# Kernel tuning notes

Hardware: AMD Instinct MI355X
Metric: run time of the kernel (lower is better)

Reference implementation:

```python
import jax, jax.numpy as jnp
import numpy as np
from jax import lax

HEADS = 8
EPS = 1e-5
B, HP, N = 16, 16, 256  # batch, patches per side, tokens


def _ln(x, w, b):
    m = x.mean(-1, keepdims=True)
    v = ((x - m) ** 2).mean(-1, keepdims=True)
    return (x - m) / jnp.sqrt(v + EPS) * w + b


def _mlp_block(x, n2w, n2b, f1w, f1b, f2w, f2b):
    h = _ln(x, n2w, n2b)
    h = jax.nn.gelu(h @ f1w.T + f1b, approximate=False)  # torch nn.GELU = exact erf
    return x + (h @ f2w.T + f2b)


def _stem_stage(x, params):
    def step(c, p):
        return _mlp_block(c, *p), None
    x, _ = lax.scan(step, x, params)
    return x


def _patch_merge(x, nw, nb, rw):
    # x: [B, N, s, s, C] -> [B, N, s/2, s/2, 2C]
    x = jnp.concatenate([x[..., 0::2, 0::2, :], x[..., 1::2, 0::2, :],
                         x[..., 0::2, 1::2, :], x[..., 1::2, 1::2, :]], axis=-1)
    return _ln(x, nw, nb) @ rw.T


def _main_block(x, p, rpe_index):
    n1w, n1b, qkvw, qkvb, rpb, pw, pb, n2w, n2b, f1w, f1b, f2w, f2b = p
    Bc, Nc, C = x.shape
    Dh = C // HEADS
    h = _ln(x, n1w, n1b)
    qkv = (h @ qkvw.T + qkvb).reshape(Bc, Nc, 3, HEADS, Dh)
    q, k, v = jnp.moveaxis(qkv, 2, 0)
    attn = jnp.einsum('bnhd,bmhd->bhnm', q * (Dh ** -0.5), k)
    # learned relative position bias gathered per (query, key) pair
    bias = rpb[rpe_index].reshape(Nc, Nc, HEADS).transpose(2, 0, 1)  # [H,N,N]
    attn = jax.nn.softmax((attn + bias[None]).astype(jnp.float32), axis=-1).astype(x.dtype)
    o = jnp.einsum('bhnm,bmhd->bnhd', attn, v).reshape(Bc, Nc, C)
    x = x + (o @ pw.T + pb)
    return _mlp_block(x, n2w, n2b, f1w, f1b, f2w, f2b)


def _forward(x, patch_w, patch_b, pnorm_w, pnorm_b,
             s0_n2w, s0_n2b, s0_fc1w, s0_fc1b, s0_fc2w, s0_fc2b,
             m0_nw, m0_nb, m0_rw,
             s1_n2w, s1_n2b, s1_fc1w, s1_fc1b, s1_fc2w, s1_fc2b,
             m1_nw, m1_nb, m1_rw, pos_embed,
             mb_n1w, mb_n1b, mb_qkvw, mb_qkvb, mb_rpb, mb_projw, mb_projb,
             mb_n2w, mb_n2b, mb_fc1w, mb_fc1b, mb_fc2w, mb_fc2b,
             fnorm_w, fnorm_b, rpe_index):
    Bc = x.shape[0]
    # PatchEmbed: 4x4/stride4 conv, regroup into [B, 256 patches, 4, 4, 128]
    h = lax.conv_general_dilated(x, patch_w, (4, 4), 'VALID',
                                 dimension_numbers=('NCHW', 'OIHW', 'NCHW'))
    h = h + patch_b[None, :, None, None]  # [B,128,64,64]
    h = h.reshape(Bc, 128, HP, 4, HP, 4).transpose(0, 2, 4, 3, 5, 1).reshape(Bc, N, 4, 4, 128)
    h = _ln(h, pnorm_w, pnorm_b)
    # stem stage 0 (8 MLP-only blocks, dim 128) + merge -> dim 256
    h = _stem_stage(h, (s0_n2w, s0_n2b, s0_fc1w, s0_fc1b, s0_fc2w, s0_fc2b))
    h = _patch_merge(h, m0_nw, m0_nb, m0_rw)  # [B,256,2,2,256]
    # stem stage 1 (8 MLP-only blocks, dim 256) + merge -> dim 512
    h = _stem_stage(h, (s1_n2w, s1_n2b, s1_fc1w, s1_fc1b, s1_fc2w, s1_fc2b))
    h = _patch_merge(h, m1_nw, m1_nb, m1_rw)  # [B,256,1,1,512]
    h = h[..., 0, 0, :] + pos_embed  # [B,256,512]
    # 20 main attention blocks with RPE
    def step(c, p):
        return _main_block(c, p, rpe_index), None
    h, _ = lax.scan(step, h, (mb_n1w, mb_n1b, mb_qkvw, mb_qkvb, mb_rpb,
                              mb_projw, mb_projb, mb_n2w, mb_n2b,
                              mb_fc1w, mb_fc1b, mb_fc2w, mb_fc2b))
    return _ln(h, fnorm_w, fnorm_b)


def _rpe_index():
    coords = np.stack(np.meshgrid(np.arange(HP), np.arange(HP), indexing='ij')).reshape(2, -1)
    rel = (coords[:, :, None] - coords[:, None, :]).transpose(1, 2, 0) + (HP - 1)
    return jnp.asarray((rel[..., 0] * (2 * HP - 1) + rel[..., 1]).reshape(-1), jnp.int32)


def setup_inputs() -> dict:
    key = jax.random.key(0)
    ks = iter(jax.random.split(key, 64))
    w = lambda shape: jax.random.normal(next(ks), shape, jnp.float32) * 0.02
    return {
        'x': jax.random.normal(next(ks), (B, 3, 256, 256), jnp.float32),
        'patch_w': w((128, 3, 4, 4)), 'patch_b': jnp.zeros(128),
        'pnorm_w': jnp.ones(128), 'pnorm_b': jnp.zeros(128),
        's0_n2w': jnp.ones((8, 128)), 's0_n2b': jnp.zeros((8, 128)),
        's0_fc1w': w((8, 384, 128)), 's0_fc1b': jnp.zeros((8, 384)),
        's0_fc2w': w((8, 128, 384)), 's0_fc2b': jnp.zeros((8, 128)),
        'm0_nw': jnp.ones(512), 'm0_nb': jnp.zeros(512), 'm0_rw': w((256, 512)),
        's1_n2w': jnp.ones((8, 256)), 's1_n2b': jnp.zeros((8, 256)),
        's1_fc1w': w((8, 768, 256)), 's1_fc1b': jnp.zeros((8, 768)),
        's1_fc2w': w((8, 256, 768)), 's1_fc2b': jnp.zeros((8, 256)),
        'm1_nw': jnp.ones(1024), 'm1_nb': jnp.zeros(1024), 'm1_rw': w((512, 1024)),
        'pos_embed': w((1, N, 512)),
        'mb_n1w': jnp.ones((20, 512)), 'mb_n1b': jnp.zeros((20, 512)),
        'mb_qkvw': w((20, 1536, 512)), 'mb_qkvb': jnp.zeros((20, 1536)),
        'mb_rpb': w((20, 961, 8)),
        'mb_projw': w((20, 512, 512)), 'mb_projb': jnp.zeros((20, 512)),
        'mb_n2w': jnp.ones((20, 512)), 'mb_n2b': jnp.zeros((20, 512)),
        'mb_fc1w': w((20, 2048, 512)), 'mb_fc1b': jnp.zeros((20, 2048)),
        'mb_fc2w': w((20, 512, 2048)), 'mb_fc2b': jnp.zeros((20, 512)),
        'fnorm_w': jnp.ones(512), 'fnorm_b': jnp.zeros(512),
        'rpe_index': _rpe_index(),
    }


def reference(x, patch_w, patch_b, pnorm_w, pnorm_b,
              s0_n2w, s0_n2b, s0_fc1w, s0_fc1b, s0_fc2w, s0_fc2b,
              m0_nw, m0_nb, m0_rw,
              s1_n2w, s1_n2b, s1_fc1w, s1_fc1b, s1_fc2w, s1_fc2b,
              m1_nw, m1_nb, m1_rw, pos_embed,
              mb_n1w, mb_n1b, mb_qkvw, mb_qkvb, mb_rpb, mb_projw, mb_projb,
              mb_n2w, mb_n2b, mb_fc1w, mb_fc1b, mb_fc2w, mb_fc2b,
              fnorm_w, fnorm_b, rpe_index):
    return _forward(x, patch_w, patch_b, pnorm_w, pnorm_b,
                    s0_n2w, s0_n2b, s0_fc1w, s0_fc1b, s0_fc2w, s0_fc2b,
                    m0_nw, m0_nb, m0_rw,
                    s1_n2w, s1_n2b, s1_fc1w, s1_fc1b, s1_fc2w, s1_fc2b,
                    m1_nw, m1_nb, m1_rw, pos_embed,
                    mb_n1w, mb_n1b, mb_qkvw, mb_qkvb, mb_rpb, mb_projw, mb_projb,
                    mb_n2w, mb_n2b, mb_fc1w, mb_fc1b, mb_fc2w, mb_fc2b,
                    fnorm_w, fnorm_b, rpe_index)
```

## Files before the change

### kernel.cpp

```cpp
#include <hip/hip_runtime.h>
#include <math.h>

#define EPSV 1e-5f

typedef __attribute__((ext_vector_type(8))) short bf16x8;
typedef __attribute__((ext_vector_type(4))) float f32x4;
typedef unsigned short ushort;

__device__ inline ushort f2bf(float x) {
  unsigned u = __builtin_bit_cast(unsigned, x);
  u += 0x7FFFu + ((u >> 16) & 1u);
  return (ushort)(u >> 16);
}

#define GLOAD16(lptr, gptr)                                              \
  __builtin_amdgcn_global_load_lds(                                      \
      (const __attribute__((address_space(1))) unsigned int*)(gptr),     \
      (__attribute__((address_space(3))) unsigned int*)(lptr), 16, 0, 0)

__global__ __launch_bounds__(256) void convh_kernel(
    const float* __restrict__ in, ushort* __restrict__ hi, int n4) {
  int i = blockIdx.x * 256 + threadIdx.x;
  if (i >= n4) return;
  float4 v = ((const float4*)in)[i];
  float vv[4] = {v.x, v.y, v.z, v.w};
  unsigned hw[4];
#pragma unroll
  for (int e = 0; e < 4; ++e) hw[e] = f2bf(vv[e]);
  ((uint2*)hi)[i] = make_uint2(hw[0] | (hw[1] << 16), hw[2] | (hw[3] << 16));
}

__global__ __launch_bounds__(256) void convmain_kernel(
    const float* __restrict__ src, ushort* __restrict__ dst, int perLayer4,
    int dstOff4, int n4) {
  int i = blockIdx.x * 256 + threadIdx.x;
  if (i >= n4) return;
  int l = i / perLayer4;
  int r = i - l * perLayer4;
  float4 v = ((const float4*)src)[i];
  float vv[4] = {v.x, v.y, v.z, v.w};
  unsigned hw[4];
#pragma unroll
  for (int e = 0; e < 4; ++e) hw[e] = f2bf(vv[e]);
  ((uint2*)dst)[(size_t)l * 786432 + dstOff4 + r] =
      make_uint2(hw[0] | (hw[1] << 16), hw[2] | (hw[3] << 16));
}

__global__ __launch_bounds__(256) void patch_ln2_kernel(
    const float* __restrict__ x, const float* __restrict__ pw,
    const float* __restrict__ pbias, const float* __restrict__ nw,
    const float* __restrict__ nb, float* __restrict__ out) {
  int bid = blockIdx.x;
  int b = bid >> 8, n = bid & 255;
  int py = (n >> 4) * 16, px0 = (n & 15) * 16;
  __shared__ float xin[3][16][16];
  __shared__ float wls[128][52];
  __shared__ float pbs[128];
  int tid = threadIdx.x;
  if (tid < 192) {
    int ci = tid / 64, rr = (tid % 64) >> 2, c4 = tid & 3;
    const float* src =
        x + ((size_t)(b * 3 + ci) * 256 + (py + rr)) * 256 + px0 + c4 * 4;
    *(float4*)&xin[ci][rr][c4 * 4] = *(const float4*)src;
  }
  for (int idx = tid; idx < 6144; idx += 256) {
    int c = idx / 48, q = idx % 48;
    wls[c][q] = pw[c * 48 + q];
  }
  if (tid < 128) pbs[tid] = pbias[tid];
  __syncthreads();

  int tt = tid >> 4, cg = tid & 15;
  int ii = tt >> 2, jj = tt & 3;
  float xv[48];
#pragma unroll
  for (int ci = 0; ci < 3; ++ci)
#pragma unroll
    for (int dy = 0; dy < 4; ++dy)
#pragma unroll
      for (int dx = 0; dx < 4; ++dx)
        xv[ci * 16 + dy * 4 + dx] = xin[ci][ii * 4 + dy][jj * 4 + dx];

  float o[8];
#pragma unroll
  for (int e = 0; e < 8; ++e) {
    int c = cg + e * 16;
    float a = pbs[c];
#pragma unroll
    for (int q4 = 0; q4 < 12; ++q4) {
      float4 w4 = *(const float4*)&wls[c][q4 * 4];
      a += w4.x * xv[q4 * 4] + w4.y * xv[q4 * 4 + 1] + w4.z * xv[q4 * 4 + 2] +
           w4.w * xv[q4 * 4 + 3];
    }
    o[e] = a;
  }
  float s = 0.f;
#pragma unroll
  for (int e = 0; e < 8; ++e) s += o[e];
#pragma unroll
  for (int off = 8; off > 0; off >>= 1) s += __shfl_xor(s, off, 16);
  float mean = s * (1.0f / 128.0f);
  float sq = 0.f;
#pragma unroll
  for (int e = 0; e < 8; ++e) {
    float d = o[e] - mean;
    sq += d * d;
  }
#pragma unroll
  for (int off = 8; off > 0; off >>= 1) sq += __shfl_xor(sq, off, 16);
  float rstd = rsqrtf(sq * (1.0f / 128.0f) + EPSV);
  size_t base = ((size_t)bid * 16 + tt) * 128;
#pragma unroll
  for (int e = 0; e < 8; ++e) {
    int c = cg + e * 16;
    out[base + c] = (o[e] - mean) * rstd * nw[c] + nb[c];
  }
}

template <int C>
__global__ __launch_bounds__(256) void lnC_kernel(
    const float* __restrict__ X, const float* __restrict__ w,
    const float* __restrict__ bb, ushort* __restrict__ outH) {
  constexpr int NV = C / 64;
  int wave = threadIdx.x >> 6, lane = threadIdx.x & 63;
  int row = blockIdx.x * 4 + wave;
  const float* xr = X + (size_t)row * C + lane * NV;
  float v[NV];
  if (NV == 2) {
    float2 t2 = *(const float2*)xr;
    v[0] = t2.x; v[1] = t2.y;
  } else {
#pragma unroll
    for (int q = 0; q < NV; q += 4) {
      float4 t4 = *(const float4*)(xr + q);
      v[q] = t4.x; v[q + 1] = t4.y; v[q + 2] = t4.z; v[q + 3] = t4.w;
    }
  }
  float s = 0.f;
#pragma unroll
  for (int q = 0; q < NV; ++q) s += v[q];
#pragma unroll
  for (int o = 32; o > 0; o >>= 1) s += __shfl_xor(s, o, 64);
  float mean = s * (1.0f / C);
  float sq = 0.f;
#pragma unroll
  for (int q = 0; q < NV; ++q) {
    float d = v[q] - mean;
    sq += d * d;
  }
#pragma unroll
  for (int o = 32; o > 0; o >>= 1) sq += __shfl_xor(sq, o, 64);
  float rstd = rsqrtf(sq * (1.0f / C) + EPSV);
#pragma unroll
  for (int q = 0; q < NV; ++q) {
    int c = lane * NV + q;
    outH[(size_t)row * C + c] = f2bf((v[q] - mean) * rstd * w[c] + bb[c]);
  }
}

template <int MODE>
__global__ __launch_bounds__(256) void merge_ln_kernel(
    const float* __restrict__ Xin, const float* __restrict__ nw,
    const float* __restrict__ nb, ushort* __restrict__ outH) {
  constexpr int CM = MODE ? 1024 : 512;
  constexpr int NE = CM / 256;
  int ot = blockIdx.x;
  int tid = threadIdx.x;
  __shared__ float redA[4];
  __shared__ float redB[4];

  float v[NE];
#pragma unroll
  for (int e = 0; e < NE; ++e) {
    int cp = tid + e * 256;
    if (MODE == 0) {
      int b = ot >> 10, r = ot & 1023;
      int n = r >> 2, di = (r >> 1) & 1, dj = r & 1;
      int q = cp >> 7, c = cp & 127;
      int i = 2 * di + (q & 1), j = 2 * dj + (q >> 1);
      v[e] = Xin[((b * 256 + n) * 16 + i * 4 + j) * 128 + c];
    } else {
      int b = ot >> 8, n = ot & 255;
      int q = cp >> 8, c = cp & 255;
      int di = q & 1, dj = q >> 1;
      v[e] = Xin[((b * 256 + n) * 4 + di * 2 + dj) * 256 + c];
    }
  }
  float s = 0.f;
#pragma unroll
  for (int e = 0; e < NE; ++e) s += v[e];
#pragma unroll
  for (int o = 32; o > 0; o >>= 1) s += __shfl_xor(s, o, 64);
  if ((tid & 63) == 0) redA[tid >> 6] = s;
  __syncthreads();
  float mean = (redA[0] + redA[1] + redA[2] + redA[3]) * (1.0f / CM);
  float sq = 0.f;
#pragma unroll
  for (int e = 0; e < NE; ++e) {
    float d = v[e] - mean;
    sq += d * d;
  }
#pragma unroll
  for (int o = 32; o > 0; o >>= 1) sq += __shfl_xor(sq, o, 64);
  if ((tid & 63) == 0) redB[tid >> 6] = sq;
  __syncthreads();
  float var = (redB[0] + redB[1] + redB[2] + redB[3]) * (1.0f / CM);
  float rstd = rsqrtf(var + EPSV);
#pragma unroll
  for (int e = 0; e < NE; ++e) {
    int cp = tid + e * 256;
    outH[(size_t)ot * CM + cp] = f2bf((v[e] - mean) * rstd * nw[cp] + nb[cp]);
  }
}

template <int EP, int BM>
__global__ __launch_bounds__(256) void mgemm4_kernel(
    const ushort* __restrict__ Ah, const ushort* __restrict__ Wh,
    const float* __restrict__ bias, const float* __restrict__ extra,
    float* __restrict__ outF, ushort* __restrict__ outH, int M, int N, int K) {
  constexpr int NI = BM / 32;
  constexpr int ASH = BM * 64;
  constexpr int LSZ = (ASH + 8192 > BM * 136) ? (ASH + 8192) : (BM * 136);
  __shared__ __align__(16) ushort Lds[LSZ];
  int nb = N >> 7;
  int bx = blockIdx.x % nb, by = blockIdx.x / nb;
  int tid = threadIdx.x;
  int wv = tid >> 6, lane = tid & 63;
  int srow = tid >> 3;
  int scol = ((tid & 7) ^ (srow & 7)) << 3;
  const ushort* aS = Ah + (size_t)(by * BM + srow) * K + scol;
  const ushort* wS = Wh + (size_t)(bx * 128 + srow) * K + scol;
  ushort* dA = Lds + wv * 512;
  ushort* dW = Lds + ASH + wv * 512;

  int wm = (wv >> 1) * (BM / 2), wn = (wv & 1) * 64;
  int fr = lane & 15, fq = lane >> 4;
  int rsw = fr & 7;

  f32x4 acc[NI][4];
#pragma unroll
  for (int i = 0; i < NI; ++i)
#pragma unroll
    for (int j = 0; j < 4; ++j) acc[i][j] = {0.f, 0.f, 0.f, 0.f};

  for (int k0 = 0; k0 < K; k0 += 64) {
#pragma unroll
    for (int q = 0; q < BM / 32; ++q)
      GLOAD16(dA + q * 2048, aS + (size_t)q * 32 * K + k0);
#pragma unroll
    for (int q = 0; q < 4; ++q)
      GLOAD16(dW + q * 2048, wS + (size_t)q * 32 * K + k0);
    __syncthreads();

#pragma unroll
    for (int kh = 0; kh < 2; ++kh) {
      bf16x8 fa[NI], fb[4];
#pragma unroll
      for (int i = 0; i < NI; ++i) {
        int row = wm + i * 16 + fr;
        fa[i] = *(const bf16x8*)(Lds + row * 64 + ((((kh << 2) + fq) ^ rsw) << 3));
      }
#pragma unroll
      for (int j = 0; j < 4; ++j) {
        int row = wn + j * 16 + fr;
        fb[j] = *(const bf16x8*)(Lds + ASH + row * 64 +
                                 ((((kh << 2) + fq) ^ rsw) << 3));
      }
#pragma unroll
      for (int i = 0; i < NI; ++i)
#pragma unroll
        for (int j = 0; j < 4; ++j)
          acc[i][j] = __builtin_amdgcn_mfma_f32_16x16x32_bf16(fa[i], fb[j],
                                                              acc[i][j], 0, 0,
                                                              0);
    }
    __syncthreads();
  }

  int row0 = by * BM;
  int col0 = bx * 128;
  if (EP == 3 || EP == 4) {
    ushort* LdsO = Lds;
#pragma unroll
    for (int j = 0; j < 4; ++j) {
      int col = wn + j * 16 + fr;
      float bvv = bias ? bias[col0 + col] : 0.f;
      bool sc = (EP == 4) && (col0 + col < 512);
#pragma unroll
      for (int i = 0; i < NI; ++i) {
#pragma unroll
        for (int e = 0; e < 4; ++e) {
          int rl = wm + i * 16 + fq * 4 + e;
          float o = acc[i][j][e] + bvv;
          if (EP == 3)
            o = 0.5f * o * (1.0f + erff(o * 0.70710678118654752f));
          else if (sc)
            o *= 0.125f;
          LdsO[rl * 136 + col] = f2bf(o);
        }
      }
    }
    __syncthreads();
#pragma unroll
    for (int p = 0; p < BM / 16; ++p) {
      int ch = p * 256 + tid;
      int r = ch >> 4, cc = (ch & 15) * 8;
      *(uint4*)&outH[(size_t)(row0 + r) * N + col0 + cc] =
          *(const uint4*)&LdsO[r * 136 + cc];
    }
  } else {
    float* LdsF = (float*)Lds;
    int strip = wv >> 1;
#pragma unroll
    for (int i = 0; i < NI; ++i) {
#pragma unroll
      for (int j = 0; j < 4; ++j) {
        int col = wn + j * 16 + fr;
        float bvv = bias ? bias[col0 + col] : 0.f;
#pragma unroll
        for (int e = 0; e < 4; ++e)
          LdsF[(strip * 16 + fq * 4 + e) * 136 + col] = acc[i][j][e] + bvv;
      }
      __syncthreads();
#pragma unroll
      for (int p = 0; p < 4; ++p) {
        int c = p * 256 + tid;
        int st = c >> 9;
        int rem = c & 511;
        int r = rem >> 5, cc = (rem & 31) * 4;
        int grow = row0 + st * (BM / 2) + i * 16 + r;
        float4 v = *(const float4*)&LdsF[(st * 16 + r) * 136 + cc];
        if (EP == 1) {
          float4 e4 =
              *(const float4*)&extra[(size_t)(grow & 255) * N + col0 + cc];
          v.x += e4.x; v.y += e4.y; v.z += e4.z; v.w += e4.w;
        } else if (EP == 2) {
          float4 e4 = *(const float4*)&extra[(size_t)grow * N + col0 + cc];
          v.x += e4.x; v.y += e4.y; v.z += e4.z; v.w += e4.w;
        }
        *(float4*)&outF[(size_t)grow * N + col0 + cc] = v;
      }
      __syncthreads();
    }
  }
}

__global__ __launch_bounds__(256) void attn_score_kernel(
    const ushort* __restrict__ qkvh, const float* __restrict__ rpb,
    const int* __restrict__ rpe, ushort* __restrict__ P) {
  int bid = blockIdx.x;
  int qc = bid & 3, bh = bid >> 2;
  int b = bh >> 3, h = bh & 7;
  int n0 = qc * 64;
  int tid = threadIdx.x;
  int wv = tid >> 6, lane = tid & 63;
  int fr = lane & 15, fq = lane >> 4;
  __shared__ __align__(16) ushort Qs[64 * 64];
  __shared__ __align__(16) ushort Ks[256 * 64];
  __shared__ float rpbh[961];
  __shared__ float red[64][4];

  int srow = tid >> 3;
  int sc = ((tid & 7) ^ (srow & 7)) << 3;
  const ushort* Qg = qkvh + (size_t)(b * 256 + n0 + srow) * 1536 + h * 64 + sc;
  GLOAD16(Qs + wv * 512, Qg);
  GLOAD16(Qs + 2048 + wv * 512, Qg + (size_t)32 * 1536);
  const ushort* Kg = qkvh + (size_t)(b * 256 + srow) * 1536 + 512 + h * 64 + sc;
#pragma unroll
  for (int q = 0; q < 8; ++q)
    GLOAD16(Ks + q * 2048 + wv * 512, Kg + (size_t)q * 32 * 1536);
  for (int i = tid; i < 961; i += 256) rpbh[i] = rpb[i * 8 + h];
  __syncthreads();

  f32x4 acc[4][4];
#pragma unroll
  for (int i = 0; i < 4; ++i)
#pragma unroll
    for (int j = 0; j < 4; ++j) acc[i][j] = {0.f, 0.f, 0.f, 0.f};
#pragma unroll
  for (int kh = 0; kh < 2; ++kh) {
    bf16x8 fa[4], fb[4];
#pragma unroll
    for (int i = 0; i < 4; ++i) {
      int row = i * 16 + fr;
      fa[i] = *(const bf16x8*)(Qs + row * 64 +
                               ((((kh << 2) + fq) ^ (row & 7)) << 3));
    }
#pragma unroll
    for (int j = 0; j < 4; ++j) {
      int row = wv * 64 + j * 16 + fr;
      fb[j] = *(const bf16x8*)(Ks + row * 64 +
                               ((((kh << 2) + fq) ^ (row & 7)) << 3));
    }
#pragma unroll
    for (int i = 0; i < 4; ++i)
#pragma unroll
      for (int j = 0; j < 4; ++j)
        acc[i][j] = __builtin_amdgcn_mfma_f32_16x16x32_bf16(fa[i], fb[j],
                                                            acc[i][j], 0, 0, 0);
  }

  float sreg[4][4][4];
#pragma unroll
  for (int i = 0; i < 4; ++i)
#pragma unroll
    for (int e = 0; e < 4; ++e) {
      int n = n0 + i * 16 + fq * 4 + e;
#pragma unroll
      for (int j = 0; j < 4; ++j) {
        int m = wv * 64 + j * 16 + fr;
        sreg[i][j][e] = acc[i][j][e] + rpbh[rpe[n * 256 + m]];
      }
    }

  float rmax[4][4];
#pragma unroll
  for (int i = 0; i < 4; ++i)
#pragma unroll
    for (int e = 0; e < 4; ++e) {
      float mx = fmaxf(fmaxf(sreg[i][0][e], sreg[i][1][e]),
                       fmaxf(sreg[i][2][e], sreg[i][3][e]));
#pragma unroll
      for (int o = 8; o > 0; o >>= 1) mx = fmaxf(mx, __shfl_xor(mx, o, 16));
      if (fr == 0) red[i * 16 + fq * 4 + e][wv] = mx;
    }
  __syncthreads();
#pragma unroll
  for (int i = 0; i < 4; ++i)
#pragma unroll
    for (int e = 0; e < 4; ++e) {
      int row = i * 16 + fq * 4 + e;
      rmax[i][e] = fmaxf(fmaxf(red[row][0], red[row][1]),
                         fmaxf(red[row][2], red[row][3]));
    }
  __syncthreads();
  float rinv[4][4];
#pragma unroll
  for (int i = 0; i < 4; ++i)
#pragma unroll
    for (int e = 0; e < 4; ++e) {
      float sm = 0.f;
#pragma unroll
      for (int j = 0; j < 4; ++j) {
        sreg[i][j][e] = expf(sreg[i][j][e] - rmax[i][e]);
        sm += sreg[i][j][e];
      }
#pragma unroll
      for (int o = 8; o > 0; o >>= 1) sm += __shfl_xor(sm, o, 16);
      if (fr == 0) red[i * 16 + fq * 4 + e][wv] = sm;
    }
  __syncthreads();
#pragma unroll
  for (int i = 0; i < 4; ++i)
#pragma unroll
    for (int e = 0; e < 4; ++e) {
      int row = i * 16 + fq * 4 + e;
      rinv[i][e] =
          1.0f / (red[row][0] + red[row][1] + red[row][2] + red[row][3]);
    }
  ushort* Pr = P + ((size_t)bh * 256 + n0) * 256;
#pragma unroll
  for (int i = 0; i < 4; ++i)
#pragma unroll
    for (int e = 0; e < 4; ++e) {
      int q = i * 16 + fq * 4 + e;
#pragma unroll
      for (int j = 0; j < 4; ++j) {
        int m = wv * 64 + j * 16 + fr;
        Pr[(size_t)q * 256 + m] = f2bf(sreg[i][j][e] * rinv[i][e]);
      }
    }
}

__global__ __launch_bounds__(256) void attn_pv_kernel(
    const ushort* __restrict__ P, const ushort* __restrict__ qkvh,
    ushort* __restrict__ outH) {
  int bid = blockIdx.x;
  int qc = bid & 3, bh = bid >> 2;
  int b = bh >> 3, h = bh & 7;
  int n0 = qc * 64;
  int tid = threadIdx.x;
  int wv = tid >> 6, lane = tid & 63;
  int fr = lane & 15, fq = lane >> 4;
  __shared__ __align__(16) ushort Ps[64 * 256];
  __shared__ __align__(16) ushort Vt[64 * 256];

  {
    int srow = tid >> 5;
    int c = tid & 31;
    int cs = (c & 24) | ((c & 7) ^ (srow & 7));
    const ushort* Pg = P + ((size_t)bh * 256 + n0 + srow) * 256 + cs * 8;
#pragma unroll
    for (int q = 0; q < 8; ++q)
      GLOAD16(Ps + q * 2048 + wv * 512, Pg + (size_t)q * 8 * 256);
  }
#pragma unroll
  for (int pass = 0; pass < 4; ++pass) {
    int m = pass * 64 + (tid >> 2);
    int sg = (tid & 3) * 16;
    const ushort* Vg = qkvh + (size_t)(b * 256 + m) * 1536 + 1024 + h * 64 + sg;
    ushort tmp[16];
    *(uint4*)tmp = *(const uint4*)Vg;
    *(uint4*)(tmp + 8) = *(const uint4*)(Vg + 8);
    int ch = m >> 3, ml = m & 7;
#pragma unroll
    for (int e = 0; e < 16; ++e) {
      int d = sg + e;
      int cs = (ch & 24) | ((ch & 7) ^ (d & 7));
      Vt[d * 256 + cs * 8 + ml] = tmp[e];
    }
  }
  __syncthreads();

  f32x4 acc[4];
#pragma unroll
  for (int i = 0; i < 4; ++i) acc[i] = {0.f, 0.f, 0.f, 0.f};
  int dbase = wv * 16;
#pragma unroll
  for (int ks = 0; ks < 8; ++ks) {
    int ch = (ks << 2) + fq;
    bf16x8 fb;
    {
      int row = dbase + fr;
      int cs = (ch & 24) | ((ch & 7) ^ (row & 7));
      fb = *(const bf16x8*)(Vt + row * 256 + cs * 8);
    }
    bf16x8 fa[4];
#pragma unroll
    for (int i = 0; i < 4; ++i) {
      int row = i * 16 + fr;
      int cs = (ch & 24) | ((ch & 7) ^ (row & 7));
      fa[i] = *(const bf16x8*)(Ps + row * 256 + cs * 8);
    }
#pragma unroll
    for (int i = 0; i < 4; ++i)
      acc[i] = __builtin_amdgcn_mfma_f32_16x16x32_bf16(fa[i], fb, acc[i], 0, 0,
                                                       0);
  }
#pragma unroll
  for (int i = 0; i < 4; ++i)
#pragma unroll
    for (int e = 0; e < 4; ++e) {
      int q = i * 16 + fq * 4 + e;
      outH[(size_t)(b * 256 + n0 + q) * 512 + h * 64 + dbase + fr] =
          f2bf(acc[i][e]);
    }
}

template <int HL>
__global__ __launch_bounds__(256) void ln512_kernel(
    const float* __restrict__ X, const float* __restrict__ w,
    const float* __restrict__ bb, float* __restrict__ outF,
    ushort* __restrict__ outH) {
  int row = blockIdx.x * 4 + (threadIdx.x >> 6);
  int t = threadIdx.x & 63;
  const float4* xr = (const float4*)(X + (size_t)row * 512);
  float4 v0 = xr[t * 2], v1 = xr[t * 2 + 1];
  float s = v0.x + v0.y + v0.z + v0.w + v1.x + v1.y + v1.z + v1.w;
#pragma unroll
  for (int o = 32; o > 0; o >>= 1) s += __shfl_xor(s, o, 64);
  float mean = s * (1.0f / 512.0f);
  float dv[8] = {v0.x - mean, v0.y - mean, v0.z - mean, v0.w - mean,
                 v1.x - mean, v1.y - mean, v1.z - mean, v1.w - mean};
  float sq = 0.f;
#pragma unroll
  for (int e = 0; e < 8; ++e) sq += dv[e] * dv[e];
#pragma unroll
  for (int o = 32; o > 0; o >>= 1) sq += __shfl_xor(sq, o, 64);
  float rstd = rsqrtf(sq * (1.0f / 512.0f) + EPSV);
  int c = t * 8;
  float ov[8];
#pragma unroll
  for (int e = 0; e < 8; ++e) ov[e] = dv[e] * rstd * w[c + e] + bb[c + e];
  if (HL == 0) {
    float4 o0 = {ov[0], ov[1], ov[2], ov[3]};
    float4 o1 = {ov[4], ov[5], ov[6], ov[7]};
    ((float4*)(outF + (size_t)row * 512))[t * 2] = o0;
    ((float4*)(outF + (size_t)row * 512))[t * 2 + 1] = o1;
  } else {
    __align__(16) ushort h8[8];
#pragma unroll
    for (int e = 0; e < 8; ++e) h8[e] = f2bf(ov[e]);
    *(bf16x8*)(outH + (size_t)row * 512 + c) = *(bf16x8*)h8;
  }
}

extern "C" void kernel_launch(void* const* d_in, const int* in_sizes, int n_in,
                              void* d_out, int out_size, void* d_ws,
                              size_t ws_size, hipStream_t stream) {
  const float* x = (const float*)d_in[0];
  const float* patch_w = (const float*)d_in[1];
  const float* patch_b = (const float*)d_in[2];
  const float* pnorm_w = (const float*)d_in[3];
  const float* pnorm_b = (const float*)d_in[4];
  const float* s0_n2w = (const float*)d_in[5];
  const float* s0_n2b = (const float*)d_in[6];
  const float* s0_f1w = (const float*)d_in[7];
  const float* s0_f1b = (const float*)d_in[8];
  const float* s0_f2w = (const float*)d_in[9];
  const float* s0_f2b = (const float*)d_in[10];
  const float* m0_nw = (const float*)d_in[11];
  const float* m0_nb = (const float*)d_in[12];
  const float* m0_rw = (const float*)d_in[13];
  const float* s1_n2w = (const float*)d_in[14];
  const float* s1_n2b = (const float*)d_in[15];
  const float* s1_f1w = (const float*)d_in[16];
  const float* s1_f1b = (const float*)d_in[17];
  const float* s1_f2w = (const float*)d_in[18];
  const float* s1_f2b = (const float*)d_in[19];
  const float* m1_nw = (const float*)d_in[20];
  const float* m1_nb = (const float*)d_in[21];
  const float* m1_rw = (const float*)d_in[22];
  const float* pos_embed = (const float*)d_in[23];
  const float* mb_n1w = (const float*)d_in[24];
  const float* mb_n1b = (const float*)d_in[25];
  const float* mb_qkvw = (const float*)d_in[26];
  const float* mb_qkvb = (const float*)d_in[27];
  const float* mb_rpb = (const float*)d_in[28];
  const float* mb_projw = (const float*)d_in[29];
  const float* mb_projb = (const float*)d_in[30];
  const float* mb_n2w = (const float*)d_in[31];
  const float* mb_n2b = (const float*)d_in[32];
  const float* mb_f1w = (const float*)d_in[33];
  const float* mb_f1b = (const float*)d_in[34];
  const float* mb_f2w = (const float*)d_in[35];
  const float* mb_f2b = (const float*)d_in[36];
  const float* fnorm_w = (const float*)d_in[37];
  const float* fnorm_b = (const float*)d_in[38];
  const int* rpe = (const int*)d_in[39];

  float* Xa = (float*)d_ws;
  ushort* BufB = (ushort*)(Xa + 8388608);
  ushort* BufC = (ushort*)(Xa + 12582912);
  ushort* Qkvh = BufC;
  ushort* Ph = BufC + 6291456;
  ushort* F1h = BufC + 14680064;
  ushort* Wall = (ushort*)(Xa + 25165824);
  ushort* WallBig = (ushort*)(Xa + 27262976);

#define CONVH(src, cnt, dh)                                              \
  convh_kernel<<<((cnt) / 4 + 255) / 256, 256, 0, stream>>>(src, dh, (cnt) / 4)

  convmain_kernel<<<(20 * 196608 + 255) / 256, 256, 0, stream>>>(
      mb_qkvw, WallBig, 196608, 0, 20 * 196608);
  convmain_kernel<<<(20 * 65536 + 255) / 256, 256, 0, stream>>>(
      mb_projw, WallBig, 65536, 196608, 20 * 65536);
  convmain_kernel<<<(20 * 262144 + 255) / 256, 256, 0, stream>>>(
      mb_f1w, WallBig, 262144, 262144, 20 * 262144);
  convmain_kernel<<<(20 * 262144 + 255) / 256, 256, 0, stream>>>(
      mb_f2w, WallBig, 262144, 524288, 20 * 262144);

  patch_ln2_kernel<<<4096, 256, 0, stream>>>(x, patch_w, patch_b, pnorm_w,
                                             pnorm_b, Xa);

  CONVH(s0_f1w, 8 * 49152, Wall);
  CONVH(s0_f2w, 8 * 49152, Wall + 393216);
  for (int i = 0; i < 8; ++i) {
    lnC_kernel<128><<<65536 / 4, 256, 0, stream>>>(Xa, s0_n2w + i * 128,
                                                   s0_n2b + i * 128, BufB);
    mgemm4_kernel<3, 128><<<(65536 / 128) * (384 / 128), 256, 0, stream>>>(
        BufB, Wall + i * 49152, s0_f1b + i * 384, nullptr, nullptr, BufC,
        65536, 384, 128);
    mgemm4_kernel<2, 64><<<(65536 / 64) * (128 / 128), 256, 0, stream>>>(
        BufC, Wall + 393216 + i * 49152, s0_f2b + i * 128, Xa, Xa, nullptr,
        65536, 128, 384);
  }
  merge_ln_kernel<0><<<16384, 256, 0, stream>>>(Xa, m0_nw, m0_nb, BufB);
  CONVH(m0_rw, 131072, Wall);
  mgemm4_kernel<0, 128><<<(16384 / 128) * (256 / 128), 256, 0, stream>>>(
      BufB, Wall, nullptr, nullptr, Xa, nullptr, 16384, 256, 512);

  CONVH(s1_f1w, 8 * 196608, Wall);
  CONVH(s1_f2w, 8 * 196608, Wall + 1572864);
  for (int i = 0; i < 8; ++i) {
    lnC_kernel<256><<<16384 / 4, 256, 0, stream>>>(Xa, s1_n2w + i * 256,
                                                   s1_n2b + i * 256, BufB);
    mgemm4_kernel<3, 128><<<(16384 / 128) * (768 / 128), 256, 0, stream>>>(
        BufB, Wall + i * 196608, s1_f1b + i * 768, nullptr, nullptr, BufC,
        16384, 768, 256);
    mgemm4_kernel<2, 64><<<(16384 / 64) * (256 / 128), 256, 0, stream>>>(
        BufC, Wall + 1572864 + i * 196608, s1_f2b + i * 256, Xa, Xa, nullptr,
        16384, 256, 768);
  }
  merge_ln_kernel<1><<<4096, 256, 0, stream>>>(Xa, m1_nw, m1_nb, BufB);
  CONVH(m1_rw, 524288, Wall);
  mgemm4_kernel<1, 64><<<(4096 / 64) * (512 / 128), 256, 0, stream>>>(
      BufB, Wall, nullptr, pos_embed, Xa, nullptr, 4096, 512, 1024);

  for (int l = 0; l < 20; ++l) {
    ushort* Wl = WallBig + (size_t)l * 3145728;
    ln512_kernel<1><<<1024, 256, 0, stream>>>(Xa, mb_n1w + l * 512,
                                              mb_n1b + l * 512, nullptr, BufB);
    mgemm4_kernel<4, 128><<<(4096 / 128) * (1536 / 128), 256, 0, stream>>>(
        BufB, Wl, mb_qkvb + l * 1536, nullptr, nullptr, Qkvh, 4096, 1536,
        512);
    attn_score_kernel<<<512, 256, 0, stream>>>(Qkvh, mb_rpb + l * 7688, rpe,
                                               Ph);
    attn_pv_kernel<<<512, 256, 0, stream>>>(Ph, Qkvh, BufB);
    mgemm4_kernel<2, 64><<<(4096 / 64) * (512 / 128), 256, 0, stream>>>(
        BufB, Wl + 786432, mb_projb + l * 512, Xa, Xa, nullptr, 4096, 512,
        512);
    ln512_kernel<1><<<1024, 256, 0, stream>>>(Xa, mb_n2w + l * 512,
                                              mb_n2b + l * 512, nullptr, BufB);
    mgemm4_kernel<3, 128><<<(4096 / 128) * (2048 / 128), 256, 0, stream>>>(
        BufB, Wl + 1048576, mb_f1b + l * 2048, nullptr, nullptr, F1h, 4096,
        2048, 512);
    mgemm4_kernel<2, 64><<<(4096 / 64) * (512 / 128), 256, 0, stream>>>(
        F1h, Wl + 2097152, mb_f2b + l * 512, Xa, Xa, nullptr, 4096, 512,
        2048);
  }
  ln512_kernel<0><<<1024, 256, 0, stream>>>(Xa, fnorm_w, fnorm_b,
                                            (float*)d_out, nullptr);
}
```

Baseline: 3.730 ms.

## Fuse attention score/softmax and PV kernels, keep P in LDS

```diff
diff --git a/kernel.cpp b/kernel.cpp
--- a/kernel.cpp
+++ b/kernel.cpp
@@ -345,9 +345,9 @@
   }
 }
 
-__global__ __launch_bounds__(256) void attn_score_kernel(
+__global__ __launch_bounds__(256) void attn_fused2_kernel(
     const ushort* __restrict__ qkvh, const float* __restrict__ rpb,
-    const int* __restrict__ rpe, ushort* __restrict__ P) {
+    const int* __restrict__ rpe, ushort* __restrict__ outH) {
   int bid = blockIdx.x;
   int qc = bid & 3, bh = bid >> 2;
   int b = bh >> 3, h = bh & 7;
@@ -357,6 +357,7 @@
   int fr = lane & 15, fq = lane >> 4;
   __shared__ __align__(16) ushort Qs[64 * 64];
   __shared__ __align__(16) ushort Ks[256 * 64];
+  __shared__ __align__(16) ushort Vt[64 * 256];
   __shared__ float rpbh[961];
   __shared__ float red[64][4];
 
@@ -369,131 +370,6 @@
 #pragma unroll
   for (int q = 0; q < 8; ++q)
     GLOAD16(Ks + q * 2048 + wv * 512, Kg + (size_t)q * 32 * 1536);
-  for (int i = tid; i < 961; i += 256) rpbh[i] = rpb[i * 8 + h];
-  __syncthreads();
-
-  f32x4 acc[4][4];
-#pragma unroll
-  for (int i = 0; i < 4; ++i)
-#pragma unroll
-    for (int j = 0; j < 4; ++j) acc[i][j] = {0.f, 0.f, 0.f, 0.f};
-#pragma unroll
-  for (int kh = 0; kh < 2; ++kh) {
-    bf16x8 fa[4], fb[4];
-#pragma unroll
-    for (int i = 0; i < 4; ++i) {
-      int row = i * 16 + fr;
-      fa[i] = *(const bf16x8*)(Qs + row * 64 +
-                               ((((kh << 2) + fq) ^ (row & 7)) << 3));
-    }
-#pragma unroll
-    for (int j = 0; j < 4; ++j) {
-      int row = wv * 64 + j * 16 + fr;
-      fb[j] = *(const bf16x8*)(Ks + row * 64 +
-                               ((((kh << 2) + fq) ^ (row & 7)) << 3));
-    }
-#pragma unroll
-    for (int i = 0; i < 4; ++i)
-#pragma unroll
-      for (int j = 0; j < 4; ++j)
-        acc[i][j] = __builtin_amdgcn_mfma_f32_16x16x32_bf16(fa[i], fb[j],
-                                                            acc[i][j], 0, 0, 0);
-  }
-
-  float sreg[4][4][4];
-#pragma unroll
-  for (int i = 0; i < 4; ++i)
-#pragma unroll
-    for (int e = 0; e < 4; ++e) {
-      int n = n0 + i * 16 + fq * 4 + e;
-#pragma unroll
-      for (int j = 0; j < 4; ++j) {
-        int m = wv * 64 + j * 16 + fr;
-        sreg[i][j][e] = acc[i][j][e] + rpbh[rpe[n * 256 + m]];
-      }
-    }
-
-  float rmax[4][4];
-#pragma unroll
-  for (int i = 0; i < 4; ++i)
-#pragma unroll
-    for (int e = 0; e < 4; ++e) {
-      float mx = fmaxf(fmaxf(sreg[i][0][e], sreg[i][1][e]),
-                       fmaxf(sreg[i][2][e], sreg[i][3][e]));
-#pragma unroll
-      for (int o = 8; o > 0; o >>= 1) mx = fmaxf(mx, __shfl_xor(mx, o, 16));
-      if (fr == 0) red[i * 16 + fq * 4 + e][wv] = mx;
-    }
-  __syncthreads();
-#pragma unroll
-  for (int i = 0; i < 4; ++i)
-#pragma unroll
-    for (int e = 0; e < 4; ++e) {
-      int row = i * 16 + fq * 4 + e;
-      rmax[i][e] = fmaxf(fmaxf(red[row][0], red[row][1]),
-                         fmaxf(red[row][2], red[row][3]));
-    }
-  __syncthreads();
-  float rinv[4][4];
-#pragma unroll
-  for (int i = 0; i < 4; ++i)
-#pragma unroll
-    for (int e = 0; e < 4; ++e) {
-      float sm = 0.f;
-#pragma unroll
-      for (int j = 0; j < 4; ++j) {
-        sreg[i][j][e] = expf(sreg[i][j][e] - rmax[i][e]);
-        sm += sreg[i][j][e];
-      }
-#pragma unroll
-      for (int o = 8; o > 0; o >>= 1) sm += __shfl_xor(sm, o, 16);
-      if (fr == 0) red[i * 16 + fq * 4 + e][wv] = sm;
-    }
-  __syncthreads();
-#pragma unroll
-  for (int i = 0; i < 4; ++i)
-#pragma unroll
-    for (int e = 0; e < 4; ++e) {
-      int row = i * 16 + fq * 4 + e;
-      rinv[i][e] =
-          1.0f / (red[row][0] + red[row][1] + red[row][2] + red[row][3]);
-    }
-  ushort* Pr = P + ((size_t)bh * 256 + n0) * 256;
-#pragma unroll
-  for (int i = 0; i < 4; ++i)
-#pragma unroll
-    for (int e = 0; e < 4; ++e) {
-      int q = i * 16 + fq * 4 + e;
-#pragma unroll
-      for (int j = 0; j < 4; ++j) {
-        int m = wv * 64 + j * 16 + fr;
-        Pr[(size_t)q * 256 + m] = f2bf(sreg[i][j][e] * rinv[i][e]);
-      }
-    }
-}
-
-__global__ __launch_bounds__(256) void attn_pv_kernel(
-    const ushort* __restrict__ P, const ushort* __restrict__ qkvh,
-    ushort* __restrict__ outH) {
-  int bid = blockIdx.x;
-  int qc = bid & 3, bh = bid >> 2;
-  int b = bh >> 3, h = bh & 7;
-  int n0 = qc * 64;
-  int tid = threadIdx.x;
-  int wv = tid >> 6, lane = tid & 63;
-  int fr = lane & 15, fq = lane >> 4;
-  __shared__ __align__(16) ushort Ps[64 * 256];
-  __shared__ __align__(16) ushort Vt[64 * 256];
-
-  {
-    int srow = tid >> 5;
-    int c = tid & 31;
-    int cs = (c & 24) | ((c & 7) ^ (srow & 7));
-    const ushort* Pg = P + ((size_t)bh * 256 + n0 + srow) * 256 + cs * 8;
-#pragma unroll
-    for (int q = 0; q < 8; ++q)
-      GLOAD16(Ps + q * 2048 + wv * 512, Pg + (size_t)q * 8 * 256);
-  }
 #pragma unroll
   for (int pass = 0; pass < 4; ++pass) {
     int m = pass * 64 + (tid >> 2);
@@ -510,11 +386,114 @@
       Vt[d * 256 + cs * 8 + ml] = tmp[e];
     }
   }
-  __syncthreads();
-
-  f32x4 acc[4];
-#pragma unroll
-  for (int i = 0; i < 4; ++i) acc[i] = {0.f, 0.f, 0.f, 0.f};
+  for (int i = tid; i < 961; i += 256) rpbh[i] = rpb[i * 8 + h];
+  __syncthreads();
+
+  f32x4 acc[4][4];
+#pragma unroll
+  for (int i = 0; i < 4; ++i)
+#pragma unroll
+    for (int j = 0; j < 4; ++j) acc[i][j] = {0.f, 0.f, 0.f, 0.f};
+#pragma unroll
+  for (int kh = 0; kh < 2; ++kh) {
+    bf16x8 fa[4], fb[4];
+#pragma unroll
+    for (int i = 0; i < 4; ++i) {
+      int row = i * 16 + fr;
+      fa[i] = *(const bf16x8*)(Qs + row * 64 +
+                               ((((kh << 2) + fq) ^ (row & 7)) << 3));
+    }
+#pragma unroll
+    for (int j = 0; j < 4; ++j) {
+      int row = wv * 64 + j * 16 + fr;
+      fb[j] = *(const bf16x8*)(Ks + row * 64 +
+                               ((((kh << 2) + fq) ^ (row & 7)) << 3));
+    }
+#pragma unroll
+    for (int i = 0; i < 4; ++i)
+#pragma unroll
+      for (int j = 0; j < 4; ++j)
+        acc[i][j] = __builtin_amdgcn_mfma_f32_16x16x32_bf16(fa[i], fb[j],
+                                                            acc[i][j], 0, 0, 0);
+  }
+
+  float sreg[4][4][4];
+#pragma unroll
+  for (int i = 0; i < 4; ++i)
+#pragma unroll
+    for (int e = 0; e < 4; ++e) {
+      int n = n0 + i * 16 + fq * 4 + e;
+#pragma unroll
+      for (int j = 0; j < 4; ++j) {
+        int m = wv * 64 + j * 16 + fr;
+        sreg[i][j][e] = acc[i][j][e] + rpbh[rpe[n * 256 + m]];
+      }
+    }
+
+  float rmax[4][4];
+#pragma unroll
+  for (int i = 0; i < 4; ++i)
+#pragma unroll
+    for (int e = 0; e < 4; ++e) {
+      float mx = fmaxf(fmaxf(sreg[i][0][e], sreg[i][1][e]),
+                       fmaxf(sreg[i][2][e], sreg[i][3][e]));
+#pragma unroll
+      for (int o = 8; o > 0; o >>= 1) mx = fmaxf(mx, __shfl_xor(mx, o, 16));
+      if (fr == 0) red[i * 16 + fq * 4 + e][wv] = mx;
+    }
+  __syncthreads();
+#pragma unroll
+  for (int i = 0; i < 4; ++i)
+#pragma unroll
+    for (int e = 0; e < 4; ++e) {
+      int row = i * 16 + fq * 4 + e;
+      rmax[i][e] = fmaxf(fmaxf(red[row][0], red[row][1]),
+                         fmaxf(red[row][2], red[row][3]));
+    }
+  __syncthreads();
+  float rinv[4][4];
+#pragma unroll
+  for (int i = 0; i < 4; ++i)
+#pragma unroll
+    for (int e = 0; e < 4; ++e) {
+      float sm = 0.f;
+#pragma unroll
+      for (int j = 0; j < 4; ++j) {
+        sreg[i][j][e] = expf(sreg[i][j][e] - rmax[i][e]);
+        sm += sreg[i][j][e];
+      }
+#pragma unroll
+      for (int o = 8; o > 0; o >>= 1) sm += __shfl_xor(sm, o, 16);
+      if (fr == 0) red[i * 16 + fq * 4 + e][wv] = sm;
+    }
+  __syncthreads();
+#pragma unroll
+  for (int i = 0; i < 4; ++i)
+#pragma unroll
+    for (int e = 0; e < 4; ++e) {
+      int row = i * 16 + fq * 4 + e;
+      rinv[i][e] =
+          1.0f / (red[row][0] + red[row][1] + red[row][2] + red[row][3]);
+    }
+  ushort* Ps = Ks;
+#pragma unroll
+  for (int i = 0; i < 4; ++i)
+#pragma unroll
+    for (int e = 0; e < 4; ++e) {
+      int qrow = i * 16 + fq * 4 + e;
+#pragma unroll
+      for (int j = 0; j < 4; ++j) {
+        int m = wv * 64 + j * 16 + fr;
+        int ch = m >> 3, t = m & 7;
+        int cs = (ch & 24) | ((ch & 7) ^ (qrow & 7));
+        Ps[qrow * 256 + cs * 8 + t] = f2bf(sreg[i][j][e] * rinv[i][e]);
+      }
+    }
+  __syncthreads();
+
+  f32x4 pacc[4];
+#pragma unroll
+  for (int i = 0; i < 4; ++i) pacc[i] = {0.f, 0.f, 0.f, 0.f};
   int dbase = wv * 16;
 #pragma unroll
   for (int ks = 0; ks < 8; ++ks) {
@@ -534,8 +513,8 @@
     }
 #pragma unroll
     for (int i = 0; i < 4; ++i)
-      acc[i] = __builtin_amdgcn_mfma_f32_16x16x32_bf16(fa[i], fb, acc[i], 0, 0,
-                                                       0);
+      pacc[i] = __builtin_amdgcn_mfma_f32_16x16x32_bf16(fa[i], fb, pacc[i], 0,
+                                                        0, 0);
   }
 #pragma unroll
   for (int i = 0; i < 4; ++i)
@@ -543,7 +522,7 @@
     for (int e = 0; e < 4; ++e) {
       int q = i * 16 + fq * 4 + e;
       outH[(size_t)(b * 256 + n0 + q) * 512 + h * 64 + dbase + fr] =
-          f2bf(acc[i][e]);
+          f2bf(pacc[i][e]);
     }
 }
 
@@ -633,7 +612,6 @@
   ushort* BufB = (ushort*)(Xa + 8388608);
   ushort* BufC = (ushort*)(Xa + 12582912);
   ushort* Qkvh = BufC;
-  ushort* Ph = BufC + 6291456;
   ushort* F1h = BufC + 14680064;
   ushort* Wall = (ushort*)(Xa + 25165824);
   ushort* WallBig = (ushort*)(Xa + 27262976);
@@ -691,12 +669,11 @@
     ushort* Wl = WallBig + (size_t)l * 3145728;
     ln512_kernel<1><<<1024, 256, 0, stream>>>(Xa, mb_n1w + l * 512,
                                               mb_n1b + l * 512, nullptr, BufB);
-    mgemm4_kernel<4, 128><<<(4096 / 128) * (1536 / 128), 256, 0, stream>>>(
+    mgemm4_kernel<4, 64><<<(4096 / 64) * (1536 / 128), 256, 0, stream>>>(
         BufB, Wl, mb_qkvb + l * 1536, nullptr, nullptr, Qkvh, 4096, 1536,
         512);
-    attn_score_kernel<<<512, 256, 0, stream>>>(Qkvh, mb_rpb + l * 7688, rpe,
-                                               Ph);
-    attn_pv_kernel<<<512, 256, 0, stream>>>(Ph, Qkvh, BufB);
+    attn_fused2_kernel<<<512, 256, 0, stream>>>(Qkvh, mb_rpb + l * 7688, rpe,
+                                                BufB);
     mgemm4_kernel<2, 64><<<(4096 / 64) * (512 / 128), 256, 0, stream>>>(
         BufB, Wl + 786432, mb_projb + l * 512, Xa, Xa, nullptr, 4096, 512,
         512);
```

Result: faster. 3.531 ms, median of 2 (-5.3%).
